# Kernel tuning notes

Hardware: AMD Instinct MI355X
Metric: run time of the kernel (lower is better)

## Reference

```python
import jax, jax.numpy as jnp
import numpy as np

MARGIN = 0.2
ALPHA = 2.0
BETA = 1.5
ANGLE_THRESHOLD = 30.0
EPS_PD = 1e-6   # F.pairwise_distance eps
EPS_CS = 1e-8   # F.cosine_similarity eps
NEG_INF = -1e30
POS_INF = 1e30


def setup_inputs() -> dict:
    key = jax.random.key(0)
    k1, k2, k3 = jax.random.split(key, 3)
    B, F, A = 4096, 512, 3
    features = jax.random.normal(k1, (B, F), dtype=jnp.float32)
    labels = jax.random.randint(k2, (B,), 0, 256)
    angles = jax.random.uniform(k3, (B, A), dtype=jnp.float32) * 90.0  # degrees
    features_orig = jax.random.normal(jax.random.fold_in(key, 7), (B, F), dtype=jnp.float32)
    return {"features": features, "labels": labels, "angles": angles, "features_orig": features_orig}


def _cosine_sim_matrix(f):
    norms = jnp.linalg.norm(f, axis=1)
    denom = jnp.maximum(norms[:, None] * norms[None, :], EPS_CS)
    return (f @ f.T) / denom


def _forward(features, labels, angles, features_orig):
    B = features.shape[0]
    idx = jnp.arange(B)
    # pairwise angle distances [B,B] (torch.cdist p=2)
    adist = jnp.sqrt(jnp.sum((angles[:, None, :] - angles[None, :, :]) ** 2, axis=-1))
    same = labels[:, None] == labels[None, :]
    same = same & ~jnp.eye(B, dtype=bool)          # exclude self
    diff = labels[:, None] != labels[None, :]
    has_pos = same.any(axis=1)
    has_neg = diff.any(axis=1)
    valid = has_pos & has_neg
    # hardest positive: same label, largest angle difference
    pos_idx = jnp.argmax(jnp.where(same, adist, NEG_INF), axis=1)
    # hardest negative: among diff-label within angle threshold, most similar feature;
    # else diff-label with smallest angle difference
    sim = _cosine_sim_matrix(features)
    similar = diff & (adist < ANGLE_THRESHOLD)
    sim_any = similar.any(axis=1)
    neg_idx_hard = jnp.argmax(jnp.where(similar, sim, NEG_INF), axis=1)
    neg_idx_far = jnp.argmin(jnp.where(diff, adist, POS_INF), axis=1)
    neg_idx = jnp.where(sim_any, neg_idx_hard, neg_idx_far)
    # triplet distances (F.pairwise_distance adds eps to the diff)
    a = features
    p = features[pos_idx]
    n = features[neg_idx]
    pos_d = jnp.linalg.norm(a - p + EPS_PD, axis=1)
    neg_d = jnp.linalg.norm(a - n + EPS_PD, axis=1)
    # angle-based weights (non-differentiable, matches .item() in torch)
    pa = adist[idx, pos_idx]
    na = adist[idx, neg_idx]
    w = jnp.where(pa > 45.0, ALPHA, 1.0) * jnp.where(na < 15.0, BETA, 1.0)
    basic = jax.nn.relu(pos_d - neg_d + MARGIN)
    vmask = valid.astype(features.dtype)
    cnt = jnp.maximum(vmask.sum(), 1.0)
    triplet_loss = jnp.sum(w * basic * vmask) / cnt
    # reconstruction term
    num = jnp.sum(features * features_orig, axis=1)
    den = jnp.maximum(jnp.linalg.norm(features, axis=1) * jnp.linalg.norm(features_orig, axis=1), EPS_CS)
    recon = 1.0 - jnp.mean(num / den)
    return triplet_loss + 0.1 * recon


def reference(features, labels, angles, features_orig):
    return _forward(features, labels, angles, features_orig)
```

## Files before the change

### kernel.cpp

```cpp
#include <hip/hip_runtime.h>
#include <math.h>

#define BN 4096
#define FD 512
#define TT 128
#define BK 64
#define NJT (BN / TT)
#define NPC 64

typedef __attribute__((ext_vector_type(8))) __bf16 bf16x8;
typedef __attribute__((ext_vector_type(4))) float floatx4;
typedef unsigned long long u64;

__device__ __forceinline__ float wred_sum(float v) {
#pragma unroll
  for (int m = 1; m < 64; m <<= 1) v += __shfl_xor(v, m, 64);
  return v;
}

__device__ __forceinline__ float dot4(float4 a, float4 b) {
  return a.x * b.x + a.y * b.y + a.z * b.z + a.w * b.w;
}

__device__ __forceinline__ unsigned short f2bf(float x) {
  unsigned u = __float_as_uint(x);
  u += 0x7fffu + ((u >> 16) & 1u);
  return (unsigned short)(u >> 16);
}

__device__ __forceinline__ void load16(const void* g, void* l) {
  __builtin_amdgcn_global_load_lds(
      (const __attribute__((address_space(1))) unsigned int*)g,
      (__attribute__((address_space(3))) unsigned int*)l, 16, 0, 0);
}

__device__ __forceinline__ unsigned ford(float v) {
  unsigned u = __float_as_uint(v);
  return u ^ (((unsigned)((int)u >> 31)) | 0x80000000u);
}

template <int N>
__device__ __forceinline__ int rori(int x) {
  return __builtin_amdgcn_update_dpp(0, x, 0x120 | N, 0xf, 0xf, true);
}
template <int N>
__device__ __forceinline__ u64 ror16_u64(u64 k) {
  unsigned lo = (unsigned)rori<N>((int)(unsigned)k);
  unsigned hi = (unsigned)rori<N>((int)(unsigned)(k >> 32));
  return ((u64)hi << 32) | lo;
}
__device__ __forceinline__ u64 red16_max_u64(u64 k) {
  u64 o;
  o = ror16_u64<1>(k); k = o > k ? o : k;
  o = ror16_u64<2>(k); k = o > k ? o : k;
  o = ror16_u64<4>(k); k = o > k ? o : k;
  o = ror16_u64<8>(k); k = o > k ? o : k;
  return k;
}

__device__ __forceinline__ u64 sx64(u64 v, int m) {
  unsigned lo = (unsigned)__shfl_xor((int)(unsigned)v, m, 64);
  unsigned hi = (unsigned)__shfl_xor((int)(unsigned)(v >> 32), m, 64);
  return ((u64)hi << 32) | lo;
}

__global__ __launch_bounds__(256) void k_prep(const float* __restrict__ f,
                                              const float* __restrict__ fo,
                                              const float* __restrict__ angles,
                                              unsigned short* __restrict__ gb,
                                              float* __restrict__ rowr,
                                              float* __restrict__ ax,
                                              float* __restrict__ ay,
                                              float* __restrict__ az) {
  const int i = blockIdx.x * 4 + (threadIdx.x >> 6);
  const int lane = threadIdx.x & 63;
  const int t = blockIdx.x * 256 + threadIdx.x;
  if (t < BN) {
    ax[t] = angles[t * 3 + 0];
    ay[t] = angles[t * 3 + 1];
    az[t] = angles[t * 3 + 2];
  }
  const float4* fr = (const float4*)(f + (size_t)i * FD);
  const float4* orr = (const float4*)(fo + (size_t)i * FD);
  float4 x0 = fr[lane], x1 = fr[lane + 64];
  float4 y0 = orr[lane], y1 = orr[lane + 64];
  float sff = dot4(x0, x0) + dot4(x1, x1);
  float sfo = dot4(x0, y0) + dot4(x1, y1);
  float soo = dot4(y0, y0) + dot4(y1, y1);
  sff = wred_sum(sff);
  sfo = wred_sum(sfo);
  soo = wred_sum(soo);
  float nf = sqrtf(sff);
  float inv = 1.0f / nf;
  ushort4* gr = (ushort4*)(gb + (size_t)i * FD);
  ushort4 s0, s1;
  s0.x = f2bf(x0.x * inv); s0.y = f2bf(x0.y * inv);
  s0.z = f2bf(x0.z * inv); s0.w = f2bf(x0.w * inv);
  s1.x = f2bf(x1.x * inv); s1.y = f2bf(x1.y * inv);
  s1.z = f2bf(x1.z * inv); s1.w = f2bf(x1.w * inv);
  gr[lane] = s0;
  gr[lane + 64] = s1;
  if (lane == 0) {
    rowr[i] = sfo / fmaxf(nf * sqrtf(soo), 1e-8f);
  }
}

__global__ __launch_bounds__(256) void k_sim(const unsigned short* __restrict__ gb,
                                             const int* __restrict__ labels,
                                             const float* __restrict__ ax,
                                             const float* __restrict__ ay,
                                             const float* __restrict__ az,
                                             u64* __restrict__ pkey) {
  __shared__ unsigned short As[TT * BK];
  __shared__ unsigned short Bs[TT * BK];
  const int tid = threadIdx.x;
  const int w = tid >> 6;
  const int lane = tid & 63;
  const int wi = w >> 1, wj = w & 1;
  const int i0 = blockIdx.y * TT;
  const int j0 = blockIdx.x * TT;

  floatx4 acc[4][4];
#pragma unroll
  for (int u = 0; u < 4; u++)
#pragma unroll
    for (int v = 0; v < 4; v++) acc[u][v] = (floatx4){0.f, 0.f, 0.f, 0.f};

  const int rp = tid >> 3;
  const int q8 = ((tid & 7) ^ (rp & 7)) * 8;
  const unsigned short* gA[4];
  const unsigned short* gB[4];
  unsigned short* lA[4];
  unsigned short* lB[4];
#pragma unroll
  for (int c = 0; c < 4; c++) {
    gA[c] = gb + (size_t)(i0 + rp + 32 * c) * FD + q8;
    gB[c] = gb + (size_t)(j0 + rp + 32 * c) * FD + q8;
    lA[c] = As + (tid + 256 * c) * 8;
    lB[c] = Bs + (tid + 256 * c) * 8;
  }

  const int m = lane & 15;
  const int arow = wi * 64 + m;
  const int brow = wj * 64 + m;
  const int g4 = lane >> 4;
  const int l7 = lane & 7;
  const int koff0 = (g4 ^ l7) * 8;
  const int koff1 = ((4 + g4) ^ l7) * 8;

  for (int kc = 0; kc < FD; kc += BK) {
#pragma unroll
    for (int c = 0; c < 4; c++) {
      load16(gA[c] + kc, lA[c]);
      load16(gB[c] + kc, lB[c]);
    }
    __syncthreads();
    bf16x8 a[4], b[4];
#pragma unroll
    for (int u = 0; u < 4; u++)
      a[u] = *(const bf16x8*)(As + (arow + u * 16) * BK + koff0);
#pragma unroll
    for (int v = 0; v < 4; v++)
      b[v] = *(const bf16x8*)(Bs + (brow + v * 16) * BK + koff0);
#pragma unroll
    for (int u = 0; u < 4; u++)
#pragma unroll
      for (int v = 0; v < 4; v++)
        acc[u][v] = __builtin_amdgcn_mfma_f32_16x16x32_bf16(a[u], b[v], acc[u][v], 0, 0, 0);
#pragma unroll
    for (int u = 0; u < 4; u++)
      a[u] = *(const bf16x8*)(As + (arow + u * 16) * BK + koff1);
#pragma unroll
    for (int v = 0; v < 4; v++)
      b[v] = *(const bf16x8*)(Bs + (brow + v * 16) * BK + koff1);
#pragma unroll
    for (int u = 0; u < 4; u++)
#pragma unroll
      for (int v = 0; v < 4; v++)
        acc[u][v] = __builtin_amdgcn_mfma_f32_16x16x32_bf16(a[u], b[v], acc[u][v], 0, 0, 0);
    __syncthreads();
  }

  const int quad = lane >> 4;
  const int cx = lane & 15;
  int jc[4], lj[4];
  float jx[4], jy[4], jz[4];
#pragma unroll
  for (int v = 0; v < 4; v++) {
    jc[v] = j0 + wj * 64 + v * 16 + cx;
    lj[v] = labels[jc[v]];
    jx[v] = ax[jc[v]];
    jy[v] = ay[jc[v]];
    jz[v] = az[jc[v]];
  }
  const size_t pbase = (size_t)(blockIdx.x * 2 + wj) * BN;
#pragma unroll
  for (int u = 0; u < 4; u++) {
#pragma unroll
    for (int reg = 0; reg < 4; reg++) {
      int i = i0 + wi * 64 + u * 16 + quad * 4 + reg;
      int li = labels[i];
      float a0 = ax[i], a1 = ay[i], a2 = az[i];
      u64 key = 0;
#pragma unroll
      for (int v = 0; v < 4; v++) {
        float d0 = a0 - jx[v];
        float d1 = a1 - jy[v];
        float d2 = a2 - jz[v];
        float dd = d0 * d0 + d1 * d1 + d2 * d2;
        u64 cand = ((u64)ford(acc[u][v][reg]) << 32) | (unsigned)(~jc[v]);
        bool ok = (li != lj[v]) && (dd < 900.0f);
        if (ok && cand > key) key = cand;
      }
      key = red16_max_u64(key);
      if (cx == 0) pkey[pbase + i] = key;
    }
  }
}

__global__ __launch_bounds__(256) void k_final(const float* __restrict__ f,
                                               const int* __restrict__ labels,
                                               const float* __restrict__ ax,
                                               const float* __restrict__ ay,
                                               const float* __restrict__ az,
                                               const u64* __restrict__ pkey,
                                               float* __restrict__ rowc,
                                               float* __restrict__ rowv) {
  const int i = blockIdx.x * 4 + (threadIdx.x >> 6);
  const int lane = threadIdx.x & 63;
  const int li = labels[i];
  const float a0 = ax[i], a1 = ay[i], a2 = az[i];

  u64 keyP = 0;
  u64 keyN = ~0ull;
  const float4* ax4 = (const float4*)ax;
  const float4* ay4 = (const float4*)ay;
  const float4* az4 = (const float4*)az;
  const int4* lb4 = (const int4*)labels;
#pragma unroll
  for (int it = 0; it < 16; it++) {
    int b = it * 64 + lane;
    float4 X = ax4[b], Y = ay4[b], Z = az4[b];
    int4 L = lb4[b];
    int jb = b * 4;
#pragma unroll
    for (int s = 0; s < 4; s++) {
      float xx = s == 0 ? X.x : s == 1 ? X.y : s == 2 ? X.z : X.w;
      float yy = s == 0 ? Y.x : s == 1 ? Y.y : s == 2 ? Y.z : Y.w;
      float zz = s == 0 ? Z.x : s == 1 ? Z.y : s == 2 ? Z.z : Z.w;
      int ll = s == 0 ? L.x : s == 1 ? L.y : s == 2 ? L.z : L.w;
      int j = jb + s;
      float d0 = a0 - xx, d1 = a1 - yy, d2 = a2 - zz;
      float dd = d0 * d0 + d1 * d1 + d2 * d2;
      if (ll == li) {
        u64 kp = ((u64)__float_as_uint(dd) << 32) | (unsigned)(~j);
        if (j != i && kp > keyP) keyP = kp;
      } else {
        u64 kn = ((u64)__float_as_uint(dd) << 32) | (unsigned)j;
        if (kn < keyN) keyN = kn;
      }
    }
  }
  u64 keyS = pkey[(size_t)lane * BN + i];
#pragma unroll
  for (int off = 1; off < 64; off <<= 1) {
    u64 o = sx64(keyP, off);
    if (o > keyP) keyP = o;
    o = sx64(keyN, off);
    if (o < keyN) keyN = o;
    o = sx64(keyS, off);
    if (o > keyS) keyS = o;
  }
  bool hp = keyP != 0;
  bool hn = keyN != ~0ull;
  if (!(hp && hn)) {
    if (lane == 0) { rowc[i] = 0.0f; rowv[i] = 0.0f; }
    return;
  }
  bool sim_any = keyS != 0;
  int pos = (int)(~(unsigned)keyP);
  int neg = sim_any ? (int)(~(unsigned)keyS) : (int)(unsigned)keyN;

  const float4* fa = (const float4*)(f + (size_t)i * FD);
  const float4* fp = (const float4*)(f + (size_t)pos * FD);
  const float4* fn = (const float4*)(f + (size_t)neg * FD);
  float sp = 0.0f, sn = 0.0f;
#pragma unroll
  for (int t = 0; t < 2; t++) {
    float4 xa = fa[lane + t * 64];
    float4 xp = fp[lane + t * 64];
    float4 xn = fn[lane + t * 64];
    float dp;
    dp = xa.x - xp.x + 1e-6f; sp += dp * dp;
    dp = xa.y - xp.y + 1e-6f; sp += dp * dp;
    dp = xa.z - xp.z + 1e-6f; sp += dp * dp;
    dp = xa.w - xp.w + 1e-6f; sp += dp * dp;
    dp = xa.x - xn.x + 1e-6f; sn += dp * dp;
    dp = xa.y - xn.y + 1e-6f; sn += dp * dp;
    dp = xa.z - xn.z + 1e-6f; sn += dp * dp;
    dp = xa.w - xn.w + 1e-6f; sn += dp * dp;
  }
  sp = wred_sum(sp);
  sn = wred_sum(sn);

  if (lane == 0) {
    float pos_d = sqrtf(sp);
    float neg_d = sqrtf(sn);
    float pa = sqrtf(__uint_as_float((unsigned)(keyP >> 32)));
    float n0 = a0 - ax[neg];
    float n1 = a1 - ay[neg];
    float n2 = a2 - az[neg];
    float na = sqrtf(n0 * n0 + n1 * n1 + n2 * n2);
    float w = (pa > 45.0f ? 2.0f : 1.0f) * (na < 15.0f ? 1.5f : 1.0f);
    float basic = fmaxf(pos_d - neg_d + 0.2f, 0.0f);
    rowc[i] = w * basic;
    rowv[i] = 1.0f;
  }
}

__global__ __launch_bounds__(1024) void k_out(const float* __restrict__ rowc,
                                              const float* __restrict__ rowv,
                                              const float* __restrict__ rowr,
                                              float* __restrict__ out) {
  __shared__ float sc[16], sv[16], sr[16];
  const int t = threadIdx.x;
  float c = 0.0f, v = 0.0f, r = 0.0f;
  for (int i = t; i < BN; i += 1024) {
    c += rowc[i];
    v += rowv[i];
    r += rowr[i];
  }
  c = wred_sum(c);
  v = wred_sum(v);
  r = wred_sum(r);
  const int wid = t >> 6;
  if ((t & 63) == 0) { sc[wid] = c; sv[wid] = v; sr[wid] = r; }
  __syncthreads();
  if (t == 0) {
    float C = 0.0f, V = 0.0f, R = 0.0f;
#pragma unroll
    for (int k = 0; k < 16; k++) { C += sc[k]; V += sv[k]; R += sr[k]; }
    float tri = C / fmaxf(V, 1.0f);
    float recon = 1.0f - R / (float)BN;
    out[0] = tri + 0.1f * recon;
  }
}

extern "C" void kernel_launch(void* const* d_in, const int* in_sizes, int n_in,
                              void* d_out, int out_size, void* d_ws, size_t ws_size,
                              hipStream_t stream) {
  const float* feat = (const float*)d_in[0];
  const int* labels = (const int*)d_in[1];
  const float* angles = (const float*)d_in[2];
  const float* forig = (const float*)d_in[3];
  float* out = (float*)d_out;

  char* ws = (char*)d_ws;
  unsigned short* gb = (unsigned short*)ws;
  size_t off = (size_t)BN * FD * sizeof(unsigned short);
  u64* pkey = (u64*)(ws + off);     off += (size_t)NPC * BN * 8;
  float* rowc = (float*)(ws + off); off += (size_t)BN * 4;
  float* rowv = (float*)(ws + off); off += (size_t)BN * 4;
  float* rowr = (float*)(ws + off); off += (size_t)BN * 4;
  float* ax = (float*)(ws + off);   off += (size_t)BN * 4;
  float* ay = (float*)(ws + off);   off += (size_t)BN * 4;
  float* az = (float*)(ws + off);   off += (size_t)BN * 4;

  k_prep<<<BN / 4, 256, 0, stream>>>(feat, forig, angles, gb, rowr, ax, ay, az);
  dim3 gs(NJT, NJT);
  k_sim<<<gs, 256, 0, stream>>>(gb, labels, ax, ay, az, pkey);
  k_final<<<BN / 4, 256, 0, stream>>>(feat, labels, ax, ay, az, pkey, rowc, rowv);
  k_out<<<1, 1024, 0, stream>>>(rowc, rowv, rowr, out);
}
```

Baseline: 117.1 us.

## Exploit Gram matrix symmetry: compute upper-triangle tiles and emit row and column maxima

```diff
diff --git a/kernel.cpp b/kernel.cpp
--- a/kernel.cpp
+++ b/kernel.cpp
@@ -6,6 +6,7 @@
 #define TT 128
 #define BK 64
 #define NJT (BN / TT)
+#define NBLK (NJT * (NJT + 1) / 2)
 #define NPC 64
 
 typedef __attribute__((ext_vector_type(8))) __bf16 bf16x8;
@@ -113,12 +114,17 @@
                                              u64* __restrict__ pkey) {
   __shared__ unsigned short As[TT * BK];
   __shared__ unsigned short Bs[TT * BK];
+  int a = 0, rem = blockIdx.x;
+#pragma unroll 1
+  while (rem >= NJT - a) { rem -= NJT - a; a++; }
+  const int b = a + rem;
+  const int i0 = a * TT;
+  const int j0 = b * TT;
+
   const int tid = threadIdx.x;
   const int w = tid >> 6;
   const int lane = tid & 63;
   const int wi = w >> 1, wj = w & 1;
-  const int i0 = blockIdx.y * TT;
-  const int j0 = blockIdx.x * TT;
 
   floatx4 acc[4][4];
 #pragma unroll
@@ -155,29 +161,29 @@
       load16(gB[c] + kc, lB[c]);
     }
     __syncthreads();
-    bf16x8 a[4], b[4];
+    bf16x8 af[4], bf[4];
 #pragma unroll
     for (int u = 0; u < 4; u++)
-      a[u] = *(const bf16x8*)(As + (arow + u * 16) * BK + koff0);
+      af[u] = *(const bf16x8*)(As + (arow + u * 16) * BK + koff0);
 #pragma unroll
     for (int v = 0; v < 4; v++)
-      b[v] = *(const bf16x8*)(Bs + (brow + v * 16) * BK + koff0);
+      bf[v] = *(const bf16x8*)(Bs + (brow + v * 16) * BK + koff0);
 #pragma unroll
     for (int u = 0; u < 4; u++)
 #pragma unroll
       for (int v = 0; v < 4; v++)
-        acc[u][v] = __builtin_amdgcn_mfma_f32_16x16x32_bf16(a[u], b[v], acc[u][v], 0, 0, 0);
+        acc[u][v] = __builtin_amdgcn_mfma_f32_16x16x32_bf16(af[u], bf[v], acc[u][v], 0, 0, 0);
 #pragma unroll
     for (int u = 0; u < 4; u++)
-      a[u] = *(const bf16x8*)(As + (arow + u * 16) * BK + koff1);
+      af[u] = *(const bf16x8*)(As + (arow + u * 16) * BK + koff1);
 #pragma unroll
     for (int v = 0; v < 4; v++)
-      b[v] = *(const bf16x8*)(Bs + (brow + v * 16) * BK + koff1);
+      bf[v] = *(const bf16x8*)(Bs + (brow + v * 16) * BK + koff1);
 #pragma unroll
     for (int u = 0; u < 4; u++)
 #pragma unroll
       for (int v = 0; v < 4; v++)
-        acc[u][v] = __builtin_amdgcn_mfma_f32_16x16x32_bf16(a[u], b[v], acc[u][v], 0, 0, 0);
+        acc[u][v] = __builtin_amdgcn_mfma_f32_16x16x32_bf16(af[u], bf[v], acc[u][v], 0, 0, 0);
     __syncthreads();
   }
 
@@ -193,7 +199,8 @@
     jy[v] = ay[jc[v]];
     jz[v] = az[jc[v]];
   }
-  const size_t pbase = (size_t)(blockIdx.x * 2 + wj) * BN;
+  const size_t rbase = (size_t)(2 * b + wj) * BN;
+  u64 ckey[4] = {0, 0, 0, 0};
 #pragma unroll
   for (int u = 0; u < 4; u++) {
 #pragma unroll
@@ -201,19 +208,33 @@
       int i = i0 + wi * 64 + u * 16 + quad * 4 + reg;
       int li = labels[i];
       float a0 = ax[i], a1 = ay[i], a2 = az[i];
-      u64 key = 0;
+      u64 rkey = 0;
+      unsigned ni = (unsigned)(~i);
 #pragma unroll
       for (int v = 0; v < 4; v++) {
         float d0 = a0 - jx[v];
         float d1 = a1 - jy[v];
         float d2 = a2 - jz[v];
         float dd = d0 * d0 + d1 * d1 + d2 * d2;
-        u64 cand = ((u64)ford(acc[u][v][reg]) << 32) | (unsigned)(~jc[v]);
         bool ok = (li != lj[v]) && (dd < 900.0f);
-        if (ok && cand > key) key = cand;
+        u64 vh = (u64)ford(acc[u][v][reg]) << 32;
+        u64 candR = vh | (unsigned)(~jc[v]);
+        if (ok && candR > rkey) rkey = candR;
+        u64 candC = vh | ni;
+        if (ok && candC > ckey[v]) ckey[v] = candC;
       }
-      key = red16_max_u64(key);
-      if (cx == 0) pkey[pbase + i] = key;
+      rkey = red16_max_u64(rkey);
+      if (cx == 0) pkey[rbase + i] = rkey;
+    }
+  }
+  if (a != b) {
+    const size_t cbase = (size_t)(2 * a + wi) * BN;
+#pragma unroll
+    for (int v = 0; v < 4; v++) {
+      u64 k = ckey[v];
+      u64 o = sx64(k, 16); if (o > k) k = o;
+      o = sx64(k, 32); if (o > k) k = o;
+      if (quad == 0) pkey[cbase + jc[v]] = k;
     }
   }
 }
@@ -239,10 +260,10 @@
   const int4* lb4 = (const int4*)labels;
 #pragma unroll
   for (int it = 0; it < 16; it++) {
-    int b = it * 64 + lane;
-    float4 X = ax4[b], Y = ay4[b], Z = az4[b];
-    int4 L = lb4[b];
-    int jb = b * 4;
+    int bb = it * 64 + lane;
+    float4 X = ax4[bb], Y = ay4[bb], Z = az4[bb];
+    int4 L = lb4[bb];
+    int jb = bb * 4;
 #pragma unroll
     for (int s = 0; s < 4; s++) {
       float xx = s == 0 ? X.x : s == 1 ? X.y : s == 2 ? X.z : X.w;
@@ -367,8 +388,7 @@
   float* az = (float*)(ws + off);   off += (size_t)BN * 4;
 
   k_prep<<<BN / 4, 256, 0, stream>>>(feat, forig, angles, gb, rowr, ax, ay, az);
-  dim3 gs(NJT, NJT);
-  k_sim<<<gs, 256, 0, stream>>>(gb, labels, ax, ay, az, pkey);
+  k_sim<<<NBLK, 256, 0, stream>>>(gb, labels, ax, ay, az, pkey);
   k_final<<<BN / 4, 256, 0, stream>>>(feat, labels, ax, ay, az, pkey, rowc, rowv);
   k_out<<<1, 1024, 0, stream>>>(rowc, rowv, rowr, out);
 }
```

New measurement: 129.0 us. +10.1%, slower.
